# Kernel optimization log

Measured on AMD Instinct MI355X. Metric: run time of the kernel, lower is better.

Reference implementation:

```python
import jax, jax.numpy as jnp
import numpy as np

B, D_IN, D_H, D_OUT = 65536, 512, 512, 512
E, N_GATE, G_H = 8, 128, 128


def _glorot(key, shape):
    bound = np.sqrt(6.0 / np.prod(shape[-2:]))
    return jax.random.uniform(key, shape, jnp.float32, -bound, bound)


def setup_inputs() -> dict:
    key = jax.random.key(0)
    ks = jax.random.split(key, 10)
    inp = {
        "z": jax.random.normal(ks[0], (B, D_IN), jnp.float32),
        "idx": jnp.arange(N_GATE, dtype=jnp.int64),
        # gating MLP (nn.Linear stored as [in, out])
        "Wg1": _glorot(ks[1], (N_GATE, G_H)), "bg1": jnp.zeros((G_H,), jnp.float32),
        "Wg2": _glorot(ks[2], (G_H, G_H)), "bg2": jnp.zeros((G_H,), jnp.float32),
        "Wg3": _glorot(ks[3], (G_H, E)), "bg3": jnp.zeros((E,), jnp.float32),
        # expert layers: W [E, in, out], b [E, out]
        "W1": _glorot(ks[4], (E, D_IN, D_H)), "b1": jnp.zeros((E, D_H), jnp.float32),
        "W2": _glorot(ks[5], (E, D_H, D_H)), "b2": jnp.zeros((E, D_H), jnp.float32),
        "W3": _glorot(ks[6], (E, D_H, D_OUT)), "b3": jnp.zeros((E, D_OUT), jnp.float32),
    }
    return inp


def _expert_layer(x, w, W, b):
    # y = sum_e w[:,e] * (x @ W[e] + b[e])  -- soft dense MoE combine
    return jnp.einsum('be,bi,eio->bo', w, x, W) + w @ b


def reference(z, idx, Wg1, bg1, Wg2, bg2, Wg3, bg3, W1, b1, W2, b2, W3, b3):
    # gating MLP on selected features (eval mode: dropout is identity)
    g = jax.nn.elu(z[:, idx] @ Wg1 + bg1)
    g = jax.nn.elu(g @ Wg2 + bg2)
    w = g @ Wg3 + bg3  # raw logits, no softmax (faithful to source)
    # experts encoder
    h = jax.nn.elu(_expert_layer(z, w, W1, b1))
    h = jax.nn.elu(_expert_layer(h, w, W2, b2))
    return _expert_layer(h, w, W3, b3)
```

## Files before the change

### kernel.cpp

```cpp
#include <hip/hip_runtime.h>

#define B_ROWS 65536

typedef __attribute__((ext_vector_type(8))) __bf16 bf16x8;
typedef __attribute__((ext_vector_type(4))) float f32x4;
typedef __attribute__((ext_vector_type(8))) unsigned short u16x8;

__device__ __forceinline__ unsigned short f2bf(float f) {
  unsigned int u = __float_as_uint(f);
  u += 0x7fffu + ((u >> 16) & 1u);
  return (unsigned short)(u >> 16);
}

__device__ __forceinline__ float elu_f(float v) {
  return v > 0.f ? v : __expf(v) - 1.f;
}

__device__ __forceinline__ void async_ld16(const void* g, void* l) {
  __builtin_amdgcn_global_load_lds(
      (const __attribute__((address_space(1))) void*)g,
      (__attribute__((address_space(3))) void*)l, 16, 0, 0);
}

__global__ __launch_bounds__(256) void gating_kernel(
    const float* __restrict__ z, const int* __restrict__ idx,
    const float* __restrict__ Wg1, const float* __restrict__ bg1,
    const float* __restrict__ Wg2, const float* __restrict__ bg2,
    const float* __restrict__ Wg3, const float* __restrict__ bg3,
    float* __restrict__ wq, float* __restrict__ gscr) {
  const size_t row = (size_t)blockIdx.x * 256 + threadIdx.x;
  const float* zr = z + row * 512;
  float* g1 = gscr + row * 128;
  float* g2 = gscr + (size_t)B_ROWS * 128 + row * 128;

  for (int ct = 0; ct < 4; ct++) {
    float acc[32];
#pragma unroll
    for (int c = 0; c < 32; c++) acc[c] = bg1[ct * 32 + c];
    for (int k = 0; k < 128; k++) {
      float xv = zr[idx[k]];
      const float* wr = Wg1 + k * 128 + ct * 32;
#pragma unroll
      for (int c = 0; c < 32; c++) acc[c] += xv * wr[c];
    }
#pragma unroll
    for (int c = 0; c < 32; c++) g1[ct * 32 + c] = elu_f(acc[c]);
  }
  for (int ct = 0; ct < 4; ct++) {
    float acc[32];
#pragma unroll
    for (int c = 0; c < 32; c++) acc[c] = bg2[ct * 32 + c];
    for (int k = 0; k < 128; k++) {
      float xv = g1[k];
      const float* wr = Wg2 + k * 128 + ct * 32;
#pragma unroll
      for (int c = 0; c < 32; c++) acc[c] += xv * wr[c];
    }
#pragma unroll
    for (int c = 0; c < 32; c++) g2[ct * 32 + c] = elu_f(acc[c]);
  }
  float a3[8];
#pragma unroll
  for (int e = 0; e < 8; e++) a3[e] = bg3[e];
  for (int k = 0; k < 128; k++) {
    float xv = g2[k];
    const float* wr = Wg3 + k * 8;
#pragma unroll
    for (int e = 0; e < 8; e++) a3[e] += xv * wr[e];
  }
#pragma unroll
  for (int e = 0; e < 8; e++) wq[row * 8 + e] = a3[e];
}

__global__ __launch_bounds__(256) void convert_bf16_k(
    const float* __restrict__ in, unsigned short* __restrict__ out) {
  size_t i = ((size_t)blockIdx.x * 256 + threadIdx.x) * 8;
  float4 a = *(const float4*)(in + i);
  float4 b = *(const float4*)(in + i + 4);
  u16x8 r;
  r[0] = f2bf(a.x); r[1] = f2bf(a.y); r[2] = f2bf(a.z); r[3] = f2bf(a.w);
  r[4] = f2bf(b.x); r[5] = f2bf(b.y); r[6] = f2bf(b.z); r[7] = f2bf(b.w);
  *(u16x8*)(out + i) = r;
}

__global__ __launch_bounds__(256) void transpose_w(
    const float* __restrict__ W1, const float* __restrict__ W2,
    const float* __restrict__ W3, unsigned short* __restrict__ Wt) {
  __shared__ float t[32][33];
  const int le = blockIdx.z;
  const float* W = (le < 8) ? W1 : (le < 16) ? W2 : W3;
  const size_t eoff = (size_t)(le & 7) * 262144;
  unsigned short* O = Wt + (size_t)le * 262144;
  const int i0 = blockIdx.y * 32, o0 = blockIdx.x * 32;
  const int tx = threadIdx.x & 31, ty = threadIdx.x >> 5;
#pragma unroll
  for (int s = 0; s < 4; s++)
    t[ty + s * 8][tx] = W[eoff + (size_t)(i0 + ty + s * 8) * 512 + o0 + tx];
  __syncthreads();
#pragma unroll
  for (int s = 0; s < 4; s++)
    O[(size_t)(o0 + ty + s * 8) * 512 + i0 + tx] = f2bf(t[tx][ty + s * 8]);
}

template <bool ELU, bool OUTBF>
__global__ __launch_bounds__(256, 2) void expert_layer(
    const unsigned short* __restrict__ X,
    const unsigned short* __restrict__ Wt,
    const float* __restrict__ bias,
    const float* __restrict__ wq,
    void* __restrict__ Out) {
  __shared__ short a_tile[128 * 64];
  __shared__ short b_tile[128 * 64];
  __shared__ float w_lds[8 * 128];
  __shared__ float bias_lds[8 * 128];

  const int tid = threadIdx.x;
  const int lane = tid & 63;
  const int wave = tid >> 6;
  const int wr = wave >> 1, wc = wave & 1;
  const int lhi = lane >> 4, llo = lane & 15;

  const int g = blockIdx.x;
  const int xcd = g & 7;
  const int s = g >> 3;
  const int nb = s & 3;
  const int mb = xcd * 64 + (s >> 2);
  const size_t row0 = (size_t)mb * 128;
  const int col0 = nb * 128;

  for (int i = tid; i < 1024; i += 256) {
    const int e = i >> 7, r = i & 127;
    w_lds[i] = wq[(row0 + r) * 8 + e];
    bias_lds[i] = bias[e * 512 + col0 + r];
  }

  const int srow = tid >> 3;
  const int cgo = ((tid & 7) ^ (srow & 7)) << 4;
  const char* Ab = (const char*)X + (row0 + srow) * 1024 + cgo;
  const char* Bb = (const char*)Wt + (size_t)(col0 + srow) * 1024 + cgo;
  char* aL = (char*)a_tile + tid * 16;
  char* bL = (char*)b_tile + tid * 16;

  const f32x4 vzero = {0.f, 0.f, 0.f, 0.f};
  f32x4 C[4][4];
#pragma unroll
  for (int i = 0; i < 4; i++)
#pragma unroll
    for (int j = 0; j < 4; j++) C[i][j] = vzero;

  const int rsw = llo & 7;

  for (int e = 0; e < 8; e++) {
    f32x4 acc[4][4];
#pragma unroll
    for (int i = 0; i < 4; i++)
#pragma unroll
      for (int j = 0; j < 4; j++) acc[i][j] = vzero;
    const char* Be = Bb + (size_t)e * 524288;
    for (int kt = 0; kt < 8; kt++) {
      const char* ga = Ab + kt * 128;
      const char* gb = Be + kt * 128;
#pragma unroll
      for (int j = 0; j < 4; j++) {
        async_ld16(ga + j * 32768, aL + j * 4096);
        async_ld16(gb + j * 32768, bL + j * 4096);
      }
      __syncthreads();
#pragma unroll
      for (int ks = 0; ks < 2; ks++) {
        const int slot = (ks * 4 + lhi) ^ rsw;
        bf16x8 av[4], bv[4];
#pragma unroll
        for (int fm = 0; fm < 4; fm++)
          av[fm] = *(const bf16x8*)((const char*)a_tile +
                                    (wr * 64 + fm * 16 + llo) * 128 + slot * 16);
#pragma unroll
        for (int fn = 0; fn < 4; fn++)
          bv[fn] = *(const bf16x8*)((const char*)b_tile +
                                    (wc * 64 + fn * 16 + llo) * 128 + slot * 16);
#pragma unroll
        for (int fm = 0; fm < 4; fm++)
#pragma unroll
          for (int fn = 0; fn < 4; fn++)
            acc[fm][fn] = __builtin_amdgcn_mfma_f32_16x16x32_bf16(
                av[fm], bv[fn], acc[fm][fn], 0, 0, 0);
      }
      __syncthreads();
    }
#pragma unroll
    for (int fm = 0; fm < 4; fm++) {
      const f32x4 wv =
          *(const f32x4*)(w_lds + e * 128 + wr * 64 + fm * 16 + lhi * 4);
#pragma unroll
      for (int fn = 0; fn < 4; fn++)
#pragma unroll
        for (int r = 0; r < 4; r++) C[fm][fn][r] += wv[r] * acc[fm][fn][r];
    }
  }

#pragma unroll
  for (int e = 0; e < 8; e++) {
    f32x4 wv[4];
#pragma unroll
    for (int fm = 0; fm < 4; fm++)
      wv[fm] = *(const f32x4*)(w_lds + e * 128 + wr * 64 + fm * 16 + lhi * 4);
#pragma unroll
    for (int fn = 0; fn < 4; fn++) {
      const float bb = bias_lds[e * 128 + wc * 64 + fn * 16 + llo];
#pragma unroll
      for (int fm = 0; fm < 4; fm++)
#pragma unroll
        for (int r = 0; r < 4; r++) C[fm][fn][r] += wv[fm][r] * bb;
    }
  }

#pragma unroll
  for (int fm = 0; fm < 4; fm++)
#pragma unroll
    for (int fn = 0; fn < 4; fn++)
#pragma unroll
      for (int r = 0; r < 4; r++) {
        float v = C[fm][fn][r];
        if (ELU) v = elu_f(v);
        const size_t orow = row0 + wr * 64 + fm * 16 + lhi * 4 + r;
        const int ocol = col0 + wc * 64 + fn * 16 + llo;
        if (OUTBF)
          ((unsigned short*)Out)[orow * 512 + ocol] = f2bf(v);
        else
          ((float*)Out)[orow * 512 + ocol] = v;
      }
}

extern "C" void kernel_launch(void* const* d_in, const int* in_sizes, int n_in,
                              void* d_out, int out_size, void* d_ws,
                              size_t ws_size, hipStream_t stream) {
  (void)in_sizes; (void)n_in; (void)out_size; (void)ws_size;
  const float* z   = (const float*)d_in[0];
  const int*   idx = (const int*)d_in[1];
  const float* Wg1 = (const float*)d_in[2];
  const float* bg1 = (const float*)d_in[3];
  const float* Wg2 = (const float*)d_in[4];
  const float* bg2 = (const float*)d_in[5];
  const float* Wg3 = (const float*)d_in[6];
  const float* bg3 = (const float*)d_in[7];
  const float* W1  = (const float*)d_in[8];
  const float* b1  = (const float*)d_in[9];
  const float* W2  = (const float*)d_in[10];
  const float* b2  = (const float*)d_in[11];
  const float* W3  = (const float*)d_in[12];
  const float* b3  = (const float*)d_in[13];

  char* ws = (char*)d_ws;
  float* wq = (float*)ws;
  unsigned short* zb = (unsigned short*)(ws + (size_t)(2u << 20));
  unsigned short* h1 = (unsigned short*)(ws + (size_t)(66u << 20));
  unsigned short* Wt = (unsigned short*)(ws + (size_t)(130u << 20));
  float* gscr = (float*)h1;
  unsigned short* h2 = zb;

  gating_kernel<<<dim3(256), dim3(256), 0, stream>>>(
      z, idx, Wg1, bg1, Wg2, bg2, Wg3, bg3, wq, gscr);
  convert_bf16_k<<<dim3(16384), dim3(256), 0, stream>>>(z, zb);
  transpose_w<<<dim3(16, 16, 24), dim3(256), 0, stream>>>(W1, W2, W3, Wt);

  expert_layer<true, true><<<dim3(2048), dim3(256), 0, stream>>>(
      zb, Wt, b1, wq, (void*)h1);
  expert_layer<true, true><<<dim3(2048), dim3(256), 0, stream>>>(
      h1, Wt + (size_t)8 * 262144, b2, wq, (void*)h2);
  expert_layer<false, false><<<dim3(2048), dim3(256), 0, stream>>>(
      h2, Wt + (size_t)16 * 262144, b3, wq, d_out);
}
```

Before: 1.406 ms.

## Compute gating MLP with fp16 MFMA tiles and fuse bf16 conversion of z

Replaces the scalar per-thread gating MLP, which spilled intermediates to a global scratch buffer, with a block-tiled kernel. Each block stages 128 rows of gathered inputs and the transposed weights in LDS and runs all three layers on fp16 MFMA instructions. The separate z-to-bf16 conversion kernel is folded into the same kernel, removing one launch and the scratch round-trip. In exchange, the gating activations now run in fp16 precision, and every block re-reads and re-converts the gating weights.

```diff
diff --git a/kernel.cpp b/kernel.cpp
--- a/kernel.cpp
+++ b/kernel.cpp
@@ -3,6 +3,7 @@
 #define B_ROWS 65536
 
 typedef __attribute__((ext_vector_type(8))) __bf16 bf16x8;
+typedef __attribute__((ext_vector_type(8))) _Float16 f16x8;
 typedef __attribute__((ext_vector_type(4))) float f32x4;
 typedef __attribute__((ext_vector_type(8))) unsigned short u16x8;
 
@@ -22,65 +23,152 @@
       (__attribute__((address_space(3))) void*)l, 16, 0, 0);
 }
 
-__global__ __launch_bounds__(256) void gating_kernel(
+#define GP 136
+
+__global__ __launch_bounds__(256) void gating_mfma(
     const float* __restrict__ z, const int* __restrict__ idx,
     const float* __restrict__ Wg1, const float* __restrict__ bg1,
     const float* __restrict__ Wg2, const float* __restrict__ bg2,
     const float* __restrict__ Wg3, const float* __restrict__ bg3,
-    float* __restrict__ wq, float* __restrict__ gscr) {
-  const size_t row = (size_t)blockIdx.x * 256 + threadIdx.x;
-  const float* zr = z + row * 512;
-  float* g1 = gscr + row * 128;
-  float* g2 = gscr + (size_t)B_ROWS * 128 + row * 128;
-
-  for (int ct = 0; ct < 4; ct++) {
-    float acc[32];
-#pragma unroll
-    for (int c = 0; c < 32; c++) acc[c] = bg1[ct * 32 + c];
-    for (int k = 0; k < 128; k++) {
-      float xv = zr[idx[k]];
-      const float* wr = Wg1 + k * 128 + ct * 32;
-#pragma unroll
-      for (int c = 0; c < 32; c++) acc[c] += xv * wr[c];
-    }
-#pragma unroll
-    for (int c = 0; c < 32; c++) g1[ct * 32 + c] = elu_f(acc[c]);
-  }
-  for (int ct = 0; ct < 4; ct++) {
-    float acc[32];
-#pragma unroll
-    for (int c = 0; c < 32; c++) acc[c] = bg2[ct * 32 + c];
-    for (int k = 0; k < 128; k++) {
-      float xv = g1[k];
-      const float* wr = Wg2 + k * 128 + ct * 32;
-#pragma unroll
-      for (int c = 0; c < 32; c++) acc[c] += xv * wr[c];
-    }
-#pragma unroll
-    for (int c = 0; c < 32; c++) g2[ct * 32 + c] = elu_f(acc[c]);
-  }
-  float a3[8];
-#pragma unroll
-  for (int e = 0; e < 8; e++) a3[e] = bg3[e];
-  for (int k = 0; k < 128; k++) {
-    float xv = g2[k];
-    const float* wr = Wg3 + k * 8;
-#pragma unroll
-    for (int e = 0; e < 8; e++) a3[e] += xv * wr[e];
-  }
-#pragma unroll
-  for (int e = 0; e < 8; e++) wq[row * 8 + e] = a3[e];
-}
-
-__global__ __launch_bounds__(256) void convert_bf16_k(
-    const float* __restrict__ in, unsigned short* __restrict__ out) {
-  size_t i = ((size_t)blockIdx.x * 256 + threadIdx.x) * 8;
-  float4 a = *(const float4*)(in + i);
-  float4 b = *(const float4*)(in + i + 4);
-  u16x8 r;
-  r[0] = f2bf(a.x); r[1] = f2bf(a.y); r[2] = f2bf(a.z); r[3] = f2bf(a.w);
-  r[4] = f2bf(b.x); r[5] = f2bf(b.y); r[6] = f2bf(b.z); r[7] = f2bf(b.w);
-  *(u16x8*)(out + i) = r;
+    float* __restrict__ wq, unsigned short* __restrict__ zb) {
+  __shared__ _Float16 Ab[128 * GP];
+  __shared__ _Float16 Wb[128 * GP];
+  __shared__ int idx_l[128];
+
+  const int tid = threadIdx.x;
+  const int lane = tid & 63, wave = tid >> 6;
+  const int wr = wave >> 1, wc = wave & 1;
+  const int lhi = lane >> 4, llo = lane & 15;
+  const size_t row0 = (size_t)blockIdx.x * 128;
+
+  if (tid < 128) idx_l[tid] = idx[tid];
+  for (int i = tid; i < 16384; i += 256) {
+    const int k = i >> 7, n = i & 127;
+    Wb[n * GP + k] = (_Float16)Wg1[i];
+  }
+  {
+    const float* zr = z + row0 * 512;
+    unsigned short* zo = zb + row0 * 512;
+    for (int i = tid; i < 8192; i += 256) {
+      const size_t off = (size_t)i * 8;
+      float4 a = *(const float4*)(zr + off);
+      float4 b = *(const float4*)(zr + off + 4);
+      u16x8 r;
+      r[0] = f2bf(a.x); r[1] = f2bf(a.y); r[2] = f2bf(a.z); r[3] = f2bf(a.w);
+      r[4] = f2bf(b.x); r[5] = f2bf(b.y); r[6] = f2bf(b.z); r[7] = f2bf(b.w);
+      *(u16x8*)(zo + off) = r;
+    }
+  }
+  __syncthreads();
+  for (int i = tid; i < 16384; i += 256) {
+    const int r = i >> 7, c = i & 127;
+    Ab[r * GP + c] = (_Float16)z[(row0 + r) * 512 + idx_l[c]];
+  }
+  __syncthreads();
+
+  const f32x4 vzero = {0.f, 0.f, 0.f, 0.f};
+
+  f32x4 C[4][4];
+#pragma unroll
+  for (int i = 0; i < 4; i++)
+#pragma unroll
+    for (int j = 0; j < 4; j++) C[i][j] = vzero;
+#pragma unroll
+  for (int ks = 0; ks < 4; ks++) {
+    f16x8 av[4], bv[4];
+#pragma unroll
+    for (int fm = 0; fm < 4; fm++)
+      av[fm] = *(const f16x8*)&Ab[(wr * 64 + fm * 16 + llo) * GP + ks * 32 + lhi * 8];
+#pragma unroll
+    for (int fn = 0; fn < 4; fn++)
+      bv[fn] = *(const f16x8*)&Wb[(wc * 64 + fn * 16 + llo) * GP + ks * 32 + lhi * 8];
+#pragma unroll
+    for (int fm = 0; fm < 4; fm++)
+#pragma unroll
+      for (int fn = 0; fn < 4; fn++)
+        C[fm][fn] = __builtin_amdgcn_mfma_f32_16x16x32_f16(av[fm], bv[fn], C[fm][fn], 0, 0, 0);
+  }
+  __syncthreads();
+#pragma unroll
+  for (int fm = 0; fm < 4; fm++)
+#pragma unroll
+    for (int fn = 0; fn < 4; fn++) {
+      const int col = wc * 64 + fn * 16 + llo;
+      const float bb = bg1[col];
+#pragma unroll
+      for (int r = 0; r < 4; r++) {
+        const int row = wr * 64 + fm * 16 + lhi * 4 + r;
+        Ab[row * GP + col] = (_Float16)elu_f(C[fm][fn][r] + bb);
+      }
+    }
+  for (int i = tid; i < 16384; i += 256) {
+    const int k = i >> 7, n = i & 127;
+    Wb[n * GP + k] = (_Float16)Wg2[i];
+  }
+  __syncthreads();
+
+#pragma unroll
+  for (int i = 0; i < 4; i++)
+#pragma unroll
+    for (int j = 0; j < 4; j++) C[i][j] = vzero;
+#pragma unroll
+  for (int ks = 0; ks < 4; ks++) {
+    f16x8 av[4], bv[4];
+#pragma unroll
+    for (int fm = 0; fm < 4; fm++)
+      av[fm] = *(const f16x8*)&Ab[(wr * 64 + fm * 16 + llo) * GP + ks * 32 + lhi * 8];
+#pragma unroll
+    for (int fn = 0; fn < 4; fn++)
+      bv[fn] = *(const f16x8*)&Wb[(wc * 64 + fn * 16 + llo) * GP + ks * 32 + lhi * 8];
+#pragma unroll
+    for (int fm = 0; fm < 4; fm++)
+#pragma unroll
+      for (int fn = 0; fn < 4; fn++)
+        C[fm][fn] = __builtin_amdgcn_mfma_f32_16x16x32_f16(av[fm], bv[fn], C[fm][fn], 0, 0, 0);
+  }
+  __syncthreads();
+#pragma unroll
+  for (int fm = 0; fm < 4; fm++)
+#pragma unroll
+    for (int fn = 0; fn < 4; fn++) {
+      const int col = wc * 64 + fn * 16 + llo;
+      const float bb = bg2[col];
+#pragma unroll
+      for (int r = 0; r < 4; r++) {
+        const int row = wr * 64 + fm * 16 + lhi * 4 + r;
+        Ab[row * GP + col] = (_Float16)elu_f(C[fm][fn][r] + bb);
+      }
+    }
+  for (int i = tid; i < 2048; i += 256) {
+    const int k = i >> 4, n = i & 15;
+    Wb[n * GP + k] = (n < 8) ? (_Float16)Wg3[k * 8 + n] : (_Float16)0.f;
+  }
+  __syncthreads();
+
+  f32x4 C3[4];
+#pragma unroll
+  for (int i = 0; i < 4; i++) C3[i] = vzero;
+#pragma unroll
+  for (int ks = 0; ks < 4; ks++) {
+    f16x8 av[4];
+#pragma unroll
+    for (int fm = 0; fm < 4; fm++)
+      av[fm] = *(const f16x8*)&Ab[(wr * 64 + fm * 16 + llo) * GP + ks * 32 + lhi * 8];
+    const f16x8 bv = *(const f16x8*)&Wb[llo * GP + ks * 32 + lhi * 8];
+#pragma unroll
+    for (int fm = 0; fm < 4; fm++)
+      C3[fm] = __builtin_amdgcn_mfma_f32_16x16x32_f16(av[fm], bv, C3[fm], 0, 0, 0);
+  }
+  if (wc == 0 && llo < 8) {
+    const float bb = bg3[llo];
+#pragma unroll
+    for (int fm = 0; fm < 4; fm++)
+#pragma unroll
+      for (int r = 0; r < 4; r++) {
+        const size_t row = row0 + wr * 64 + fm * 16 + lhi * 4 + r;
+        wq[row * 8 + llo] = C3[fm][r] + bb;
+      }
+  }
 }
 
 __global__ __launch_bounds__(256) void transpose_w(
@@ -255,12 +343,10 @@
   unsigned short* zb = (unsigned short*)(ws + (size_t)(2u << 20));
   unsigned short* h1 = (unsigned short*)(ws + (size_t)(66u << 20));
   unsigned short* Wt = (unsigned short*)(ws + (size_t)(130u << 20));
-  float* gscr = (float*)h1;
   unsigned short* h2 = zb;
 
-  gating_kernel<<<dim3(256), dim3(256), 0, stream>>>(
-      z, idx, Wg1, bg1, Wg2, bg2, Wg3, bg3, wq, gscr);
-  convert_bf16_k<<<dim3(16384), dim3(256), 0, stream>>>(z, zb);
+  gating_mfma<<<dim3(512), dim3(256), 0, stream>>>(
+      z, idx, Wg1, bg1, Wg2, bg2, Wg3, bg3, wq, zb);
   transpose_w<<<dim3(16, 16, 24), dim3(256), 0, stream>>>(W1, W2, W3, Wt);
 
   expert_layer<true, true><<<dim3(2048), dim3(256), 0, stream>>>(
```

Result: faster. 1.160 ms (-17.5%).
